# Performance work log

Hardware: AMD Instinct MI355X
Metric: run time of the kernel (lower is better)

Reference implementation:

```python
import jax, jax.numpy as jnp
import numpy as np

NUM_CLASSES = 60
FEATURE_DIM = 256
SEQ_LEN = 128
NUM_HEADS = 8
TOP_M = 20  # min(20, seq_len)
NUM_LAYERS = 2
EPS = 1e-5


def _layernorm(x, g, b):
    m = x.mean(-1, keepdims=True)
    v = ((x - m) ** 2).mean(-1, keepdims=True)
    return (x - m) * jax.lax.rsqrt(v + EPS) * g + b


def _topm_attention(x, qkv_w, qkv_b, proj_w, proj_b):
    # x: (B, N, C). Weights stored as (in, out) so y = x @ W + b.
    B, N, C = x.shape
    hd = C // NUM_HEADS
    scale = hd ** -0.5
    qkv = (x @ qkv_w + qkv_b).reshape(B, N, 3, NUM_HEADS, hd)
    q, k, v = (jnp.moveaxis(qkv[:, :, i], 2, 1) for i in range(3))  # (B,H,N,hd)
    s = jnp.einsum('bhnd,bhmd->bhnm', q, k) * scale  # (B,H,N,N)
    if TOP_M < N:
        # keep only per-query top-m scores (threshold at the m-th largest;
        # identical to torch scatter-mask for distinct float scores)
        kth = jax.lax.top_k(s, TOP_M)[0][..., -1:]
        s = jnp.where(s >= kth, s, -jnp.inf)
    a = jax.nn.softmax(s, axis=-1)  # dropout is identity in eval
    o = jnp.einsum('bhnm,bhmd->bhnd', a, v)
    o = o.transpose(0, 2, 1, 3).reshape(B, N, C)
    return o @ proj_w + proj_b


def setup_inputs() -> dict:
    key = jax.random.key(0)
    ks = jax.random.split(key, 20)
    B = 8 * NUM_CLASSES
    C = FEATURE_DIM
    d = {
        'reweighted_features': jax.random.normal(ks[0], (B, C, SEQ_LEN), jnp.float32),
        'pos_embed': jax.random.normal(ks[1], (1, SEQ_LEN, C), jnp.float32) * 0.02,
        'cls_w1': jax.random.normal(ks[2], (C, C // 2), jnp.float32) / np.sqrt(C),
        'cls_b1': jnp.zeros((C // 2,), jnp.float32),
        'cls_w2': jax.random.normal(ks[3], (C // 2, 1), jnp.float32) / np.sqrt(C // 2),
        'cls_b2': jnp.zeros((1,), jnp.float32),
    }
    for i in range(NUM_LAYERS):
        d[f'qkv_w{i}'] = jax.random.normal(ks[4 + 4 * i], (C, 3 * C), jnp.float32) / np.sqrt(C)
        d[f'qkv_b{i}'] = jnp.zeros((3 * C,), jnp.float32)
        d[f'proj_w{i}'] = jax.random.normal(ks[5 + 4 * i], (C, C), jnp.float32) / np.sqrt(C)
        d[f'proj_b{i}'] = jnp.zeros((C,), jnp.float32)
        d[f'ln_g{i}'] = jnp.ones((C,), jnp.float32)
        d[f'ln_b{i}'] = jnp.zeros((C,), jnp.float32)
    return d


def reference(reweighted_features, pos_embed, cls_w1, cls_b1, cls_w2, cls_b2,
              qkv_w0, qkv_b0, proj_w0, proj_b0, ln_g0, ln_b0,
              qkv_w1, qkv_b1, proj_w1, proj_b1, ln_g1, ln_b1):
    B = reweighted_features.shape[0] // NUM_CLASSES
    x = reweighted_features.transpose(0, 2, 1)  # (B*cls, N, C)
    x = x + pos_embed
    layers = [(qkv_w0, qkv_b0, proj_w0, proj_b0, ln_g0, ln_b0),
              (qkv_w1, qkv_b1, proj_w1, proj_b1, ln_g1, ln_b1)]
    for qw, qb, pw, pb, g, b in layers:
        x = _layernorm(x + _topm_attention(x, qw, qb, pw, pb), g, b)
    x = x.mean(axis=1)  # (B*cls, C)
    x = x.reshape(B, NUM_CLASSES, FEATURE_DIM)
    h = jax.nn.relu(x @ cls_w1 + cls_b1)  # dropout identity in eval
    logits = (h @ cls_w2 + cls_b2).reshape(B, NUM_CLASSES)
    return logits
```

## Files before the change

### kernel.cpp

```cpp
#include <hip/hip_runtime.h>
#include <hip/hip_bf16.h>
#include <cmath>

#define NSEQ 480
#define SEQN 128
#define CDIM 256
#define NH 8
#define HD 32
#define TOPM 20

typedef float f32x4 __attribute__((ext_vector_type(4)));
typedef short bf16x8 __attribute__((ext_vector_type(8)));

__device__ __forceinline__ unsigned short bf16_rn(float x) {
    unsigned int u = __float_as_uint(x);
    unsigned int r = (u + 0x7FFFu + ((u >> 16) & 1u)) >> 16;
    return (unsigned short)r;
}
__device__ __forceinline__ float bf16f(unsigned short h) {
    return __uint_as_float(((unsigned int)h) << 16);
}
__device__ __forceinline__ unsigned int okey(float v) {
    unsigned int u = __float_as_uint(v);
    return (u >> 31) ? ~u : (u | 0x80000000u);
}
__device__ __forceinline__ float okey_inv(unsigned int k) {
    return __uint_as_float((k >> 31) ? (k & 0x7FFFFFFFu) : ~k);
}
__device__ __forceinline__ unsigned pk_bf16(float a, float b) {
    union { __hip_bfloat162 h; unsigned u; } cv;
    cv.h = __float22bfloat162_rn(make_float2(a, b));
    return cv.u;
}

__global__ __launch_bounds__(256) void prep_kernel(const float* __restrict__ RW,
                                                   const float* __restrict__ POS,
                                                   unsigned short* __restrict__ XH,
                                                   unsigned short* __restrict__ XL) {
    int b = blockIdx.x, n0 = blockIdx.y * 32, c0 = blockIdx.z * 32;
    __shared__ float tile[32][33];
    int tx = threadIdx.x & 31, ty = threadIdx.x >> 5;
#pragma unroll
    for (int jj = 0; jj < 4; ++jj) {
        int c = c0 + ty + 8 * jj;
        tile[ty + 8 * jj][tx] = RW[((size_t)b * CDIM + c) * SEQN + n0 + tx];
    }
    __syncthreads();
#pragma unroll
    for (int jj = 0; jj < 4; ++jj) {
        int n = n0 + ty + 8 * jj;
        int c = c0 + tx;
        float val = tile[tx][ty + 8 * jj] + POS[n * CDIM + c];
        unsigned short hi = bf16_rn(val);
        size_t idx = (size_t)b * SEQN * CDIM + n * CDIM + c;
        XH[idx] = hi;
        XL[idx] = bf16_rn(val - bf16f(hi));
    }
}

__global__ __launch_bounds__(256) void wsplit_kernel(const float* __restrict__ W,
                                                     unsigned short* __restrict__ WtHi,
                                                     unsigned short* __restrict__ WtLo) {
    int k0 = blockIdx.x * 32, j0 = blockIdx.y * 32;
    __shared__ float tile[32][33];
    int tx = threadIdx.x & 31, ty = threadIdx.x >> 5;
#pragma unroll
    for (int jj = 0; jj < 4; ++jj)
        tile[ty + 8 * jj][tx] = W[(size_t)(k0 + ty + 8 * jj) * 768 + j0 + tx];
    __syncthreads();
#pragma unroll
    for (int jj = 0; jj < 4; ++jj) {
        float v = tile[tx][ty + 8 * jj];
        unsigned short hi = bf16_rn(v);
        unsigned short lo = bf16_rn(v - bf16f(hi));
        size_t idx = (size_t)(j0 + ty + 8 * jj) * 256 + k0 + tx;
        WtHi[idx] = hi;
        WtLo[idx] = lo;
    }
}

__global__ __launch_bounds__(256, 4) void attn_kernel(
    const unsigned short* __restrict__ XHi, const unsigned short* __restrict__ XLo,
    float* __restrict__ O,
    const unsigned short* __restrict__ WtHi, const unsigned short* __restrict__ WtLo,
    const float* __restrict__ BIAS) {
    const int bid = blockIdx.x;
    const int h = (bid >> 3) & 7;
    const int b = ((bid >> 6) << 3) | (bid & 7);
    const float scale = 0.17677669529663687f;

    __shared__ unsigned short qh[SEQN * HD], ql[SEQN * HD];
    __shared__ unsigned short kh[SEQN * HD], kl[SEQN * HD];
    __shared__ unsigned short vh[HD * SEQN];

    const int tid = threadIdx.x;
    const int w = tid >> 6;
    const int l = tid & 63;
    const int l15 = l & 15;
    const int sct = l >> 4;
    const size_t xbase = (size_t)b * SEQN * CDIM;

    f32x4 acc[2][6];
#pragma unroll
    for (int mi = 0; mi < 2; ++mi)
#pragma unroll
        for (int ni = 0; ni < 6; ++ni) acc[mi][ni] = (f32x4){0.f, 0.f, 0.f, 0.f};

#pragma unroll 2
    for (int ks = 0; ks < 8; ++ks) {
        const int kb = ks * 32;
        bf16x8 ahi[2], alo[2];
#pragma unroll
        for (int mi = 0; mi < 2; ++mi) {
            int row = w * 32 + mi * 16 + l15;
            size_t off = xbase + row * CDIM + kb + sct * 8;
            ahi[mi] = *reinterpret_cast<const bf16x8*>(XHi + off);
            alo[mi] = *reinterpret_cast<const bf16x8*>(XLo + off);
        }
#pragma unroll
        for (int ni = 0; ni < 6; ++ni) {
            int j = ((ni >> 1) << 8) + h * HD + ((ni & 1) << 4) + l15;
            const int woff = j * 256 + kb + sct * 8;
            bf16x8 bh = *reinterpret_cast<const bf16x8*>(WtHi + woff);
            if (ni < 4) {
                bf16x8 bl = *reinterpret_cast<const bf16x8*>(WtLo + woff);
#pragma unroll
                for (int mi = 0; mi < 2; ++mi) {
                    acc[mi][ni] = __builtin_amdgcn_mfma_f32_16x16x32_bf16(ahi[mi], bh, acc[mi][ni], 0, 0, 0);
                    acc[mi][ni] = __builtin_amdgcn_mfma_f32_16x16x32_bf16(ahi[mi], bl, acc[mi][ni], 0, 0, 0);
                    acc[mi][ni] = __builtin_amdgcn_mfma_f32_16x16x32_bf16(alo[mi], bh, acc[mi][ni], 0, 0, 0);
                }
            } else {
#pragma unroll
                for (int mi = 0; mi < 2; ++mi)
                    acc[mi][ni] = __builtin_amdgcn_mfma_f32_16x16x32_bf16(ahi[mi], bh, acc[mi][ni], 0, 0, 0);
            }
        }
    }
#pragma unroll
    for (int ni = 0; ni < 6; ++ni) {
        const int sel = ni >> 1;
        const int dcol = ((ni & 1) << 4) + l15;
        const float bias = BIAS[(sel << 8) + h * HD + dcol];
#pragma unroll
        for (int mi = 0; mi < 2; ++mi) {
            const int tb = w * 32 + mi * 16 + sct * 4;
            if (sel == 2) {
                float v0 = acc[mi][ni][0] + bias, v1 = acc[mi][ni][1] + bias;
                float v2 = acc[mi][ni][2] + bias, v3 = acc[mi][ni][3] + bias;
                unsigned pA = pk_bf16(v0, v1), pB = pk_bf16(v2, v3);
                int c0i = tb ^ ((dcol & 7) << 3);
                *reinterpret_cast<uint2*>(&vh[dcol * SEQN + c0i]) = make_uint2(pA, pB);
            } else {
                unsigned short* ph = sel ? kh : qh;
                unsigned short* pl = sel ? kl : ql;
#pragma unroll
                for (int r = 0; r < 4; ++r) {
                    float v = acc[mi][ni][r] + bias;
                    if (sel == 0) v *= scale;
                    unsigned short hi = bf16_rn(v);
                    int token = tb + r;
                    int idx = token * HD + (dcol ^ (((token >> 1) & 3) << 3));
                    ph[idx] = hi;
                    pl[idx] = bf16_rn(v - bf16f(hi));
                }
            }
        }
    }
    __syncthreads();

    f32x4 sacc[8][2];
#pragma unroll
    for (int mi = 0; mi < 8; ++mi)
#pragma unroll
        for (int ni = 0; ni < 2; ++ni) sacc[mi][ni] = (f32x4){0.f, 0.f, 0.f, 0.f};

    bf16x8 qfh[2], qfl[2];
#pragma unroll
    for (int ni = 0; ni < 2; ++ni) {
        int qrow = w * 32 + (ni << 4) + l15;
        int off = qrow * HD + ((sct * 8) ^ (((qrow >> 1) & 3) << 3));
        qfh[ni] = *reinterpret_cast<const bf16x8*>(qh + off);
        qfl[ni] = *reinterpret_cast<const bf16x8*>(ql + off);
    }
#pragma unroll
    for (int mi = 0; mi < 8; ++mi) {
        int krow = (mi << 4) + l15;
        int off = krow * HD + ((sct * 8) ^ (((krow >> 1) & 3) << 3));
        bf16x8 kfh = *reinterpret_cast<const bf16x8*>(kh + off);
        bf16x8 kfl = *reinterpret_cast<const bf16x8*>(kl + off);
#pragma unroll
        for (int ni = 0; ni < 2; ++ni) {
            sacc[mi][ni] = __builtin_amdgcn_mfma_f32_16x16x32_bf16(kfh, qfh[ni], sacc[mi][ni], 0, 0, 0);
            sacc[mi][ni] = __builtin_amdgcn_mfma_f32_16x16x32_bf16(kfh, qfl[ni], sacc[mi][ni], 0, 0, 0);
            sacc[mi][ni] = __builtin_amdgcn_mfma_f32_16x16x32_bf16(kfl, qfh[ni], sacc[mi][ni], 0, 0, 0);
        }
    }
#pragma unroll
    for (int mi = 0; mi < 8; ++mi)
#pragma unroll
        for (int ni = 0; ni < 2; ++ni)
#pragma unroll
            for (int r = 0; r < 4; ++r)
                sacc[mi][ni][r] = __uint_as_float(okey(sacc[mi][ni][r]));

    unsigned int p0 = 0u, p1 = 0u;
    for (int bit = 31; bit >= 0; --bit) {
        unsigned int t0 = p0 | (1u << bit), t1 = p1 | (1u << bit);
        int c0 = 0, c1 = 0;
#pragma unroll
        for (int mi = 0; mi < 8; ++mi)
#pragma unroll
            for (int r = 0; r < 4; ++r) {
                c0 += (__float_as_uint(sacc[mi][0][r]) >= t0) ? 1 : 0;
                c1 += (__float_as_uint(sacc[mi][1][r]) >= t1) ? 1 : 0;
            }
        int m = c0 | (c1 << 8);
        m += __shfl_xor(m, 16);
        m += __shfl_xor(m, 32);
        if ((m & 255) >= TOPM) p0 = t0;
        if ((m >> 8) >= TOPM) p1 = t1;
    }
    unsigned int km0 = 0u, km1 = 0u;
#pragma unroll
    for (int mi = 0; mi < 8; ++mi)
#pragma unroll
        for (int r = 0; r < 4; ++r) {
            km0 = max(km0, __float_as_uint(sacc[mi][0][r]));
            km1 = max(km1, __float_as_uint(sacc[mi][1][r]));
        }
    km0 = max(km0, (unsigned int)__shfl_xor((int)km0, 16));
    km0 = max(km0, (unsigned int)__shfl_xor((int)km0, 32));
    km1 = max(km1, (unsigned int)__shfl_xor((int)km1, 16));
    km1 = max(km1, (unsigned int)__shfl_xor((int)km1, 32));
    float mx0 = okey_inv(km0), mx1 = okey_inv(km1);

    float s0 = 0.f, s1 = 0.f;
#pragma unroll
    for (int mi = 0; mi < 8; ++mi)
#pragma unroll
        for (int r = 0; r < 4; ++r) {
            unsigned int u0 = __float_as_uint(sacc[mi][0][r]);
            unsigned int u1 = __float_as_uint(sacc[mi][1][r]);
            float e0 = (u0 >= p0) ? __expf(okey_inv(u0) - mx0) : 0.f;
            float e1 = (u1 >= p1) ? __expf(okey_inv(u1) - mx1) : 0.f;
            sacc[mi][0][r] = e0;
            sacc[mi][1][r] = e1;
            s0 += e0;
            s1 += e1;
        }
    s0 += __shfl_xor(s0, 16);
    s0 += __shfl_xor(s0, 32);
    s1 += __shfl_xor(s1, 16);
    s1 += __shfl_xor(s1, 32);
    float i0 = 1.f / s0, i1 = 1.f / s1;

    unsigned w16[8][2][2];
#pragma unroll
    for (int mi = 0; mi < 8; ++mi)
#pragma unroll
        for (int ni = 0; ni < 2; ++ni)
#pragma unroll
            for (int p = 0; p < 2; ++p)
                w16[mi][ni][p] = pk_bf16(sacc[mi][ni][2 * p], sacc[mi][ni][2 * p + 1]);

    f32x4 oacc[2][2];
#pragma unroll
    for (int mi = 0; mi < 2; ++mi)
#pragma unroll
        for (int ni = 0; ni < 2; ++ni) oacc[mi][ni] = (f32x4){0.f, 0.f, 0.f, 0.f};

#pragma unroll
    for (int k = 0; k < 4; ++k) {
        bf16x8 bvh[2];
#pragma unroll
        for (int nio = 0; nio < 2; ++nio) {
            int drow = (nio << 4) + l15;
            int off = drow * SEQN + ((k * 32 + sct * 8) ^ ((drow & 7) << 3));
            bvh[nio] = *reinterpret_cast<const bf16x8*>(vh + off);
        }
#pragma unroll
        for (int mio = 0; mio < 2; ++mio) {
            union { unsigned u[4]; bf16x8 v8; } aw;
#pragma unroll
            for (int j = 0; j < 4; ++j) {
                int src = l15 + ((sct & 1) << 5) + ((j >> 1) << 4);
                unsigned a0 = (unsigned)__shfl((int)w16[2 * k][mio][j & 1], src);
                unsigned a1 = (unsigned)__shfl((int)w16[2 * k + 1][mio][j & 1], src);
                aw.u[j] = (sct >= 2) ? a1 : a0;
            }
#pragma unroll
            for (int nio = 0; nio < 2; ++nio)
                oacc[mio][nio] = __builtin_amdgcn_mfma_f32_16x16x32_bf16(aw.v8, bvh[nio], oacc[mio][nio], 0, 0, 0);
        }
    }
    float invO[2][4];
#pragma unroll
    for (int mio = 0; mio < 2; ++mio)
#pragma unroll
        for (int r = 0; r < 4; ++r)
            invO[mio][r] = __shfl(mio ? i1 : i0, sct * 4 + r);
#pragma unroll
    for (int mio = 0; mio < 2; ++mio)
#pragma unroll
        for (int nio = 0; nio < 2; ++nio)
#pragma unroll
            for (int r = 0; r < 4; ++r) {
                int token = w * 32 + mio * 16 + sct * 4 + r;
                int d = (nio << 4) + l15;
                O[((size_t)b * SEQN + token) * CDIM + h * HD + d] = oacc[mio][nio][r] * invO[mio][r];
            }
}

__global__ __launch_bounds__(256) void projln_kernel(const float* __restrict__ O,
                                                     unsigned short* __restrict__ XH,
                                                     unsigned short* __restrict__ XL,
                                                     const float* __restrict__ W,
                                                     const float* __restrict__ PB,
                                                     const float* __restrict__ G,
                                                     const float* __restrict__ BB) {
    int b = blockIdx.x;
    int t0 = blockIdx.y * 16;
    __shared__ float T[16 * 256];
    __shared__ float red[2][16][16];
    __shared__ float mstat[16], rstdv[16];
    int tid = threadIdx.x;

#pragma unroll
    for (int ii = 0; ii < 16; ++ii) {
        int e = tid + 256 * ii;
        T[e] = O[((size_t)b * SEQN + t0 + (e >> 8)) * CDIM + (e & 255)];
    }
    __syncthreads();

    int j = tid;
    float acc[16];
#pragma unroll
    for (int i = 0; i < 16; ++i) acc[i] = 0.f;
    for (int k = 0; k < CDIM; ++k) {
        float w = W[k * CDIM + j];
#pragma unroll
        for (int i = 0; i < 16; ++i) acc[i] = fmaf(T[i * 256 + k], w, acc[i]);
    }
    float bias = PB[j];
    float vals[16];
#pragma unroll
    for (int i = 0; i < 16; ++i) {
        size_t idx = ((size_t)b * SEQN + t0 + i) * CDIM + j;
        float res = bf16f(XH[idx]) + bf16f(XL[idx]);
        vals[i] = acc[i] + bias + res;
    }
    __syncthreads();
#pragma unroll
    for (int i = 0; i < 16; ++i) T[i * 256 + j] = vals[i];
    __syncthreads();
    {
        int i2 = tid >> 4, sidx = tid & 15;
        float ps = 0.f, pq = 0.f;
#pragma unroll
        for (int t = 0; t < 16; ++t) {
            float u = T[i2 * 256 + sidx * 16 + t];
            ps += u;
            pq += u * u;
        }
        red[0][i2][sidx] = ps;
        red[1][i2][sidx] = pq;
    }
    __syncthreads();
    if (tid < 16) {
        float s1 = 0.f, s2 = 0.f;
#pragma unroll
        for (int t = 0; t < 16; ++t) { s1 += red[0][tid][t]; s2 += red[1][tid][t]; }
        float m = s1 * (1.f / 256.f);
        float var = s2 * (1.f / 256.f) - m * m;
        mstat[tid] = m;
        rstdv[tid] = rsqrtf(var + 1e-5f);
    }
    __syncthreads();
    float gj = G[j], bj = BB[j];
#pragma unroll
    for (int i = 0; i < 16; ++i) {
        float y = (vals[i] - mstat[i]) * rstdv[i] * gj + bj;
        size_t idx = ((size_t)b * SEQN + t0 + i) * CDIM + j;
        unsigned short hi = bf16_rn(y);
        XH[idx] = hi;
        XL[idx] = bf16_rn(y - bf16f(hi));
    }
}

__global__ __launch_bounds__(256) void cls_kernel(const unsigned short* __restrict__ XH,
                                                  const unsigned short* __restrict__ XL,
                                                  const float* __restrict__ W1,
                                                  const float* __restrict__ B1,
                                                  const float* __restrict__ W2,
                                                  const float* __restrict__ B2,
                                                  float* __restrict__ OUT) {
    int b = blockIdx.x;
    __shared__ float xm[256];
    __shared__ float hred[128];
    int tid = threadIdx.x;
    float sm = 0.f;
    for (int n = 0; n < SEQN; ++n) {
        size_t idx = ((size_t)b * SEQN + n) * CDIM + tid;
        sm += bf16f(XH[idx]) + bf16f(XL[idx]);
    }
    xm[tid] = sm * (1.f / 128.f);
    __syncthreads();
    if (tid < 128) {
        float a = B1[tid];
        for (int k = 0; k < CDIM; ++k) a = fmaf(xm[k], W1[k * 128 + tid], a);
        a = fmaxf(a, 0.f);
        hred[tid] = a * W2[tid];
    }
    __syncthreads();
    for (int off = 64; off > 0; off >>= 1) {
        if (tid < off) hred[tid] += hred[tid + off];
        __syncthreads();
    }
    if (tid == 0) OUT[b] = hred[0] + B2[0];
}

extern "C" void kernel_launch(void* const* d_in, const int* in_sizes, int n_in,
                              void* d_out, int out_size, void* d_ws, size_t ws_size,
                              hipStream_t stream) {
    const float* RW  = (const float*)d_in[0];
    const float* POS = (const float*)d_in[1];
    const float* CW1 = (const float*)d_in[2];
    const float* CB1 = (const float*)d_in[3];
    const float* CW2 = (const float*)d_in[4];
    const float* CB2 = (const float*)d_in[5];

    const size_t NTOK = (size_t)NSEQ * SEQN * CDIM;
    float* O = (float*)d_ws;
    unsigned short* XH = (unsigned short*)(O + NTOK);
    unsigned short* XL = XH + NTOK;
    unsigned short* WtHi = XL + NTOK;
    unsigned short* WtLo = WtHi + (size_t)768 * 256;

    prep_kernel<<<dim3(NSEQ, 4, 8), 256, 0, stream>>>(RW, POS, XH, XL);

    for (int li = 0; li < 2; ++li) {
        const float* qw = (const float*)d_in[6 + 6 * li];
        const float* qb = (const float*)d_in[7 + 6 * li];
        const float* pw = (const float*)d_in[8 + 6 * li];
        const float* pb = (const float*)d_in[9 + 6 * li];
        const float* lg = (const float*)d_in[10 + 6 * li];
        const float* lb = (const float*)d_in[11 + 6 * li];
        wsplit_kernel<<<dim3(8, 24), 256, 0, stream>>>(qw, WtHi, WtLo);
        attn_kernel<<<NSEQ * NH, 256, 0, stream>>>(XH, XL, O, WtHi, WtLo, qb);
        projln_kernel<<<dim3(NSEQ, 8), 256, 0, stream>>>(O, XH, XL, pw, pb, lg, lb);
    }

    cls_kernel<<<NSEQ, 256, 0, stream>>>(XH, XL, CW1, CB1, CW2, CB2, (float*)d_out);
}
```

Baseline: 860.3 us.

## Move output projection to split-bf16 MFMA and use early-exit top-k bisection

```diff
diff --git a/kernel.cpp b/kernel.cpp
--- a/kernel.cpp
+++ b/kernel.cpp
@@ -31,6 +31,12 @@
     union { __hip_bfloat162 h; unsigned u; } cv;
     cv.h = __float22bfloat162_rn(make_float2(a, b));
     return cv.u;
+}
+__device__ __forceinline__ void unpack_bf16x8(uint4 u, float* o) {
+    o[0] = bf16f((unsigned short)(u.x & 0xffffu)); o[1] = bf16f((unsigned short)(u.x >> 16));
+    o[2] = bf16f((unsigned short)(u.y & 0xffffu)); o[3] = bf16f((unsigned short)(u.y >> 16));
+    o[4] = bf16f((unsigned short)(u.z & 0xffffu)); o[5] = bf16f((unsigned short)(u.z >> 16));
+    o[6] = bf16f((unsigned short)(u.w & 0xffffu)); o[7] = bf16f((unsigned short)(u.w >> 16));
 }
 
 __global__ __launch_bounds__(256) void prep_kernel(const float* __restrict__ RW,
@@ -60,13 +66,14 @@
 
 __global__ __launch_bounds__(256) void wsplit_kernel(const float* __restrict__ W,
                                                      unsigned short* __restrict__ WtHi,
-                                                     unsigned short* __restrict__ WtLo) {
+                                                     unsigned short* __restrict__ WtLo,
+                                                     int ncols) {
     int k0 = blockIdx.x * 32, j0 = blockIdx.y * 32;
     __shared__ float tile[32][33];
     int tx = threadIdx.x & 31, ty = threadIdx.x >> 5;
 #pragma unroll
     for (int jj = 0; jj < 4; ++jj)
-        tile[ty + 8 * jj][tx] = W[(size_t)(k0 + ty + 8 * jj) * 768 + j0 + tx];
+        tile[ty + 8 * jj][tx] = W[(size_t)(k0 + ty + 8 * jj) * ncols + j0 + tx];
     __syncthreads();
 #pragma unroll
     for (int jj = 0; jj < 4; ++jj) {
@@ -81,7 +88,7 @@
 
 __global__ __launch_bounds__(256, 4) void attn_kernel(
     const unsigned short* __restrict__ XHi, const unsigned short* __restrict__ XLo,
-    float* __restrict__ O,
+    unsigned short* __restrict__ OH, unsigned short* __restrict__ OL,
     const unsigned short* __restrict__ WtHi, const unsigned short* __restrict__ WtLo,
     const float* __restrict__ BIAS) {
     const int bid = blockIdx.x;
@@ -204,23 +211,6 @@
             for (int r = 0; r < 4; ++r)
                 sacc[mi][ni][r] = __uint_as_float(okey(sacc[mi][ni][r]));
 
-    unsigned int p0 = 0u, p1 = 0u;
-    for (int bit = 31; bit >= 0; --bit) {
-        unsigned int t0 = p0 | (1u << bit), t1 = p1 | (1u << bit);
-        int c0 = 0, c1 = 0;
-#pragma unroll
-        for (int mi = 0; mi < 8; ++mi)
-#pragma unroll
-            for (int r = 0; r < 4; ++r) {
-                c0 += (__float_as_uint(sacc[mi][0][r]) >= t0) ? 1 : 0;
-                c1 += (__float_as_uint(sacc[mi][1][r]) >= t1) ? 1 : 0;
-            }
-        int m = c0 | (c1 << 8);
-        m += __shfl_xor(m, 16);
-        m += __shfl_xor(m, 32);
-        if ((m & 255) >= TOPM) p0 = t0;
-        if ((m >> 8) >= TOPM) p1 = t1;
-    }
     unsigned int km0 = 0u, km1 = 0u;
 #pragma unroll
     for (int mi = 0; mi < 8; ++mi)
@@ -234,6 +224,45 @@
     km1 = max(km1, (unsigned int)__shfl_xor((int)km1, 16));
     km1 = max(km1, (unsigned int)__shfl_xor((int)km1, 32));
     float mx0 = okey_inv(km0), mx1 = okey_inv(km1);
+
+    unsigned p0, p1;
+    {
+        unsigned lo0 = 0u, hi0 = km0 + 1u, lo1 = 0u, hi1 = km1 + 1u;
+        unsigned th0 = km0, th1 = km1;
+        int dn0 = 0, dn1 = 0;
+#pragma unroll 1
+        for (int it = 0; it < 34; ++it) {
+            if (__all(dn0 & dn1)) break;
+            unsigned mid0 = lo0 + ((hi0 - lo0) >> 1);
+            unsigned mid1 = lo1 + ((hi1 - lo1) >> 1);
+            int c0 = 0, c1 = 0;
+#pragma unroll
+            for (int mi = 0; mi < 8; ++mi)
+#pragma unroll
+                for (int r = 0; r < 4; ++r) {
+                    c0 += (__float_as_uint(sacc[mi][0][r]) >= mid0) ? 1 : 0;
+                    c1 += (__float_as_uint(sacc[mi][1][r]) >= mid1) ? 1 : 0;
+                }
+            int mpk = c0 | (c1 << 8);
+            mpk += __shfl_xor(mpk, 16);
+            mpk += __shfl_xor(mpk, 32);
+            c0 = mpk & 255;
+            c1 = mpk >> 8;
+            if (!dn0) {
+                if (c0 == TOPM) { th0 = mid0; dn0 = 1; }
+                else if (hi0 - lo0 <= 1u) { th0 = lo0; dn0 = 1; }
+                else if (c0 > TOPM) lo0 = mid0;
+                else hi0 = mid0;
+            }
+            if (!dn1) {
+                if (c1 == TOPM) { th1 = mid1; dn1 = 1; }
+                else if (hi1 - lo1 <= 1u) { th1 = lo1; dn1 = 1; }
+                else if (c1 > TOPM) lo1 = mid1;
+                else hi1 = mid1;
+            }
+        }
+        p0 = th0; p1 = th1;
+    }
 
     float s0 = 0.f, s1 = 0.f;
 #pragma unroll
@@ -308,83 +337,129 @@
             for (int r = 0; r < 4; ++r) {
                 int token = w * 32 + mio * 16 + sct * 4 + r;
                 int d = (nio << 4) + l15;
-                O[((size_t)b * SEQN + token) * CDIM + h * HD + d] = oacc[mio][nio][r] * invO[mio][r];
-            }
-}
-
-__global__ __launch_bounds__(256) void projln_kernel(const float* __restrict__ O,
-                                                     unsigned short* __restrict__ XH,
-                                                     unsigned short* __restrict__ XL,
-                                                     const float* __restrict__ W,
-                                                     const float* __restrict__ PB,
-                                                     const float* __restrict__ G,
-                                                     const float* __restrict__ BB) {
-    int b = blockIdx.x;
-    int t0 = blockIdx.y * 16;
-    __shared__ float T[16 * 256];
-    __shared__ float red[2][16][16];
-    __shared__ float mstat[16], rstdv[16];
-    int tid = threadIdx.x;
-
-#pragma unroll
-    for (int ii = 0; ii < 16; ++ii) {
-        int e = tid + 256 * ii;
-        T[e] = O[((size_t)b * SEQN + t0 + (e >> 8)) * CDIM + (e & 255)];
-    }
-    __syncthreads();
-
-    int j = tid;
-    float acc[16];
-#pragma unroll
-    for (int i = 0; i < 16; ++i) acc[i] = 0.f;
-    for (int k = 0; k < CDIM; ++k) {
-        float w = W[k * CDIM + j];
-#pragma unroll
-        for (int i = 0; i < 16; ++i) acc[i] = fmaf(T[i * 256 + k], w, acc[i]);
-    }
-    float bias = PB[j];
-    float vals[16];
-#pragma unroll
-    for (int i = 0; i < 16; ++i) {
-        size_t idx = ((size_t)b * SEQN + t0 + i) * CDIM + j;
-        float res = bf16f(XH[idx]) + bf16f(XL[idx]);
-        vals[i] = acc[i] + bias + res;
-    }
-    __syncthreads();
-#pragma unroll
-    for (int i = 0; i < 16; ++i) T[i * 256 + j] = vals[i];
-    __syncthreads();
+                size_t idx = ((size_t)b * SEQN + token) * CDIM + h * HD + d;
+                float v = oacc[mio][nio][r] * invO[mio][r];
+                unsigned short hi = bf16_rn(v);
+                OH[idx] = hi;
+                OL[idx] = bf16_rn(v - bf16f(hi));
+            }
+}
+
+__global__ __launch_bounds__(256, 4) void projln_kernel(
+    const unsigned short* __restrict__ OHp, const unsigned short* __restrict__ OLp,
+    unsigned short* __restrict__ XH, unsigned short* __restrict__ XL,
+    const unsigned short* __restrict__ W2H, const unsigned short* __restrict__ W2L,
+    const float* __restrict__ PB, const float* __restrict__ G,
+    const float* __restrict__ BB) {
+    const int b = blockIdx.x;
+    const int t0 = blockIdx.y * 32;
+    __shared__ float vals[32 * 289];
+    __shared__ float part[8][32][2];
+
+    const int tid = threadIdx.x;
+    const int w = tid >> 6;
+    const int l = tid & 63;
+    const int l15 = l & 15;
+    const int sct = l >> 4;
+
+    f32x4 acc[2][4];
+#pragma unroll
+    for (int mi = 0; mi < 2; ++mi)
+#pragma unroll
+        for (int ni = 0; ni < 4; ++ni) acc[mi][ni] = (f32x4){0.f, 0.f, 0.f, 0.f};
+
+    const size_t obase = ((size_t)b * SEQN + t0) * CDIM;
+#pragma unroll 2
+    for (int ks = 0; ks < 8; ++ks) {
+        const int kb = ks * 32;
+        bf16x8 ahi[2], alo[2];
+#pragma unroll
+        for (int mi = 0; mi < 2; ++mi) {
+            size_t off = obase + (size_t)(mi * 16 + l15) * CDIM + kb + sct * 8;
+            ahi[mi] = *reinterpret_cast<const bf16x8*>(OHp + off);
+            alo[mi] = *reinterpret_cast<const bf16x8*>(OLp + off);
+        }
+#pragma unroll
+        for (int ni = 0; ni < 4; ++ni) {
+            int j = w * 64 + ni * 16 + l15;
+            int woff = j * 256 + kb + sct * 8;
+            bf16x8 bh = *reinterpret_cast<const bf16x8*>(W2H + woff);
+            bf16x8 bl = *reinterpret_cast<const bf16x8*>(W2L + woff);
+#pragma unroll
+            for (int mi = 0; mi < 2; ++mi) {
+                acc[mi][ni] = __builtin_amdgcn_mfma_f32_16x16x32_bf16(ahi[mi], bh, acc[mi][ni], 0, 0, 0);
+                acc[mi][ni] = __builtin_amdgcn_mfma_f32_16x16x32_bf16(ahi[mi], bl, acc[mi][ni], 0, 0, 0);
+                acc[mi][ni] = __builtin_amdgcn_mfma_f32_16x16x32_bf16(alo[mi], bh, acc[mi][ni], 0, 0, 0);
+            }
+        }
+    }
+#pragma unroll
+    for (int ni = 0; ni < 4; ++ni) {
+        int j = w * 64 + ni * 16 + l15;
+        float bias = PB[j];
+#pragma unroll
+        for (int mi = 0; mi < 2; ++mi)
+#pragma unroll
+            for (int r = 0; r < 4; ++r) {
+                int tok = mi * 16 + sct * 4 + r;
+                vals[tok * 289 + j] = acc[mi][ni][r] + bias;
+            }
+    }
+    __syncthreads();
+
+    const int row = tid & 31;
+    const int cc = tid >> 5;
+    const size_t rbase = ((size_t)b * SEQN + t0 + row) * CDIM + cc * 32;
+    float v[32];
     {
-        int i2 = tid >> 4, sidx = tid & 15;
         float ps = 0.f, pq = 0.f;
 #pragma unroll
-        for (int t = 0; t < 16; ++t) {
-            float u = T[i2 * 256 + sidx * 16 + t];
-            ps += u;
-            pq += u * u;
-        }
-        red[0][i2][sidx] = ps;
-        red[1][i2][sidx] = pq;
-    }
-    __syncthreads();
-    if (tid < 16) {
-        float s1 = 0.f, s2 = 0.f;
-#pragma unroll
-        for (int t = 0; t < 16; ++t) { s1 += red[0][tid][t]; s2 += red[1][tid][t]; }
-        float m = s1 * (1.f / 256.f);
-        float var = s2 * (1.f / 256.f) - m * m;
-        mstat[tid] = m;
-        rstdv[tid] = rsqrtf(var + 1e-5f);
-    }
-    __syncthreads();
-    float gj = G[j], bj = BB[j];
-#pragma unroll
-    for (int i = 0; i < 16; ++i) {
-        float y = (vals[i] - mstat[i]) * rstdv[i] * gj + bj;
-        size_t idx = ((size_t)b * SEQN + t0 + i) * CDIM + j;
-        unsigned short hi = bf16_rn(y);
-        XH[idx] = hi;
-        XL[idx] = bf16_rn(y - bf16f(hi));
+        for (int q = 0; q < 4; ++q) {
+            uint4 hb = *reinterpret_cast<const uint4*>(XH + rbase + q * 8);
+            uint4 lb = *reinterpret_cast<const uint4*>(XL + rbase + q * 8);
+            float rh[8], rl[8];
+            unpack_bf16x8(hb, rh);
+            unpack_bf16x8(lb, rl);
+#pragma unroll
+            for (int jj = 0; jj < 8; ++jj) {
+                int col = cc * 32 + q * 8 + jj;
+                float val = vals[row * 289 + col] + rh[jj] + rl[jj];
+                v[q * 8 + jj] = val;
+                ps += val;
+                pq = fmaf(val, val, pq);
+            }
+        }
+        part[cc][row][0] = ps;
+        part[cc][row][1] = pq;
+    }
+    __syncthreads();
+    float s1 = 0.f, s2 = 0.f;
+#pragma unroll
+    for (int k = 0; k < 8; ++k) { s1 += part[k][row][0]; s2 += part[k][row][1]; }
+    float m = s1 * (1.f / 256.f);
+    float var = s2 * (1.f / 256.f) - m * m;
+    float rstd = rsqrtf(var + 1e-5f);
+#pragma unroll
+    for (int q = 0; q < 4; ++q) {
+        int col0 = cc * 32 + q * 8;
+        float4 g0 = *reinterpret_cast<const float4*>(G + col0);
+        float4 g1 = *reinterpret_cast<const float4*>(G + col0 + 4);
+        float4 b0 = *reinterpret_cast<const float4*>(BB + col0);
+        float4 b1 = *reinterpret_cast<const float4*>(BB + col0 + 4);
+        float gg[8] = {g0.x, g0.y, g0.z, g0.w, g1.x, g1.y, g1.z, g1.w};
+        float bb2[8] = {b0.x, b0.y, b0.z, b0.w, b1.x, b1.y, b1.z, b1.w};
+        unsigned hw[4], lw[4];
+#pragma unroll
+        for (int p2 = 0; p2 < 4; ++p2) {
+            float y0 = (v[q * 8 + p2 * 2] - m) * rstd * gg[p2 * 2] + bb2[p2 * 2];
+            float y1 = (v[q * 8 + p2 * 2 + 1] - m) * rstd * gg[p2 * 2 + 1] + bb2[p2 * 2 + 1];
+            unsigned short h0 = bf16_rn(y0), h1 = bf16_rn(y1);
+            unsigned short lo0 = bf16_rn(y0 - bf16f(h0)), lo1 = bf16_rn(y1 - bf16f(h1));
+            hw[p2] = (unsigned)h0 | ((unsigned)h1 << 16);
+            lw[p2] = (unsigned)lo0 | ((unsigned)lo1 << 16);
+        }
+        *reinterpret_cast<uint4*>(XH + rbase + q * 8) = make_uint4(hw[0], hw[1], hw[2], hw[3]);
+        *reinterpret_cast<uint4*>(XL + rbase + q * 8) = make_uint4(lw[0], lw[1], lw[2], lw[3]);
     }
 }
 
@@ -431,11 +506,14 @@
     const float* CB2 = (const float*)d_in[5];
 
     const size_t NTOK = (size_t)NSEQ * SEQN * CDIM;
-    float* O = (float*)d_ws;
-    unsigned short* XH = (unsigned short*)(O + NTOK);
+    unsigned short* OH = (unsigned short*)d_ws;
+    unsigned short* OL = OH + NTOK;
+    unsigned short* XH = OL + NTOK;
     unsigned short* XL = XH + NTOK;
     unsigned short* WtHi = XL + NTOK;
     unsigned short* WtLo = WtHi + (size_t)768 * 256;
+    unsigned short* W2H = WtLo + (size_t)768 * 256;
+    unsigned short* W2L = W2H + (size_t)256 * 256;
 
     prep_kernel<<<dim3(NSEQ, 4, 8), 256, 0, stream>>>(RW, POS, XH, XL);
 
@@ -446,9 +524,10 @@
         const float* pb = (const float*)d_in[9 + 6 * li];
         const float* lg = (const float*)d_in[10 + 6 * li];
         const float* lb = (const float*)d_in[11 + 6 * li];
-        wsplit_kernel<<<dim3(8, 24), 256, 0, stream>>>(qw, WtHi, WtLo);
-        attn_kernel<<<NSEQ * NH, 256, 0, stream>>>(XH, XL, O, WtHi, WtLo, qb);
-        projln_kernel<<<dim3(NSEQ, 8), 256, 0, stream>>>(O, XH, XL, pw, pb, lg, lb);
+        wsplit_kernel<<<dim3(8, 24), 256, 0, stream>>>(qw, WtHi, WtLo, 768);
+        wsplit_kernel<<<dim3(8, 8), 256, 0, stream>>>(pw, W2H, W2L, 256);
+        attn_kernel<<<NSEQ * NH, 256, 0, stream>>>(XH, XL, OH, OL, WtHi, WtLo, qb);
+        projln_kernel<<<dim3(NSEQ, 4), 256, 0, stream>>>(OH, OL, XH, XL, W2H, W2L, pb, lg, lb);
     }
 
     cls_kernel<<<NSEQ, 256, 0, stream>>>(XH, XL, CW1, CB1, CW2, CB2, (float*)d_out);
```

Result: faster. 787.8 us (-8.4%).
